# Optimization experiments

Measured on AMD Instinct MI355X. Metric: run time of the kernel, lower is better.

## Reference

```python
import jax, jax.numpy as jnp
import numpy as np

COMMITMENT = 1.0

def setup_inputs() -> dict:
    key = jax.random.key(0)
    k1, k2 = jax.random.split(key)
    x = jax.random.normal(k1, (32, 64, 64, 64), dtype=jnp.float32)       # [B, D, H, W]
    emb_w = jax.random.normal(k2, (512, 64), dtype=jnp.float32)          # [K, D] codebook
    return {"x": x, "emb_w": emb_w}

def reference(x, emb_w):
    B, D, H, W = x.shape
    K = emb_w.shape[0]
    # permute channels last and flatten: [B*H*W, D]
    xp = jnp.transpose(x, (0, 2, 3, 1))
    flat = xp.reshape(-1, D)
    # squared-distance matrix [N, K] via ||a||^2 + ||b||^2 - 2 a.b
    distances = (jnp.sum(flat * flat, axis=1, keepdims=True)
                 + jnp.sum(emb_w * emb_w, axis=1)
                 - 2.0 * jnp.matmul(flat, emb_w.T))
    encoding_flat = jnp.argmin(distances, axis=1)                        # [N]
    quantized = emb_w[encoding_flat].reshape(B, H, W, D)                 # gather
    quantized = jnp.transpose(quantized, (0, 3, 1, 2))                   # back to [B, D, H, W]
    # commitment loss: mse(stop_grad(quantized), x)
    e_latent_loss = jnp.mean((jax.lax.stop_gradient(quantized) - x) ** 2)
    loss = COMMITMENT * e_latent_loss
    # straight-through estimator
    quantized_st = x + jax.lax.stop_gradient(quantized - x)
    encoding = encoding_flat.reshape(B, H, W)
    return quantized_st, encoding, distances, loss
```

## Files before the change

### kernel.cpp

```cpp
#include <hip/hip_runtime.h>

typedef short short8 __attribute__((ext_vector_type(8)));
typedef float f32x4 __attribute__((ext_vector_type(4)));

#define EPS 0.012f

__device__ __forceinline__ unsigned short rne_bf16(float v) {
    unsigned u = __float_as_uint(v);
    unsigned r = u + 0x7FFFu + ((u >> 16) & 1u);
    return (unsigned short)(r >> 16);
}
__device__ __forceinline__ float bf16_to_f(unsigned short h) {
    return __uint_as_float(((unsigned)h) << 16);
}

#define MFMA(a,b,c) __builtin_amdgcn_mfma_f32_16x16x32_bf16((a),(b),(c),0,0,0)

__global__ __launch_bounds__(64) void prep_kernel(
    const float* __restrict__ emb, unsigned short* __restrict__ whi,
    unsigned short* __restrict__ wlo, float* __restrict__ wee)
{
    const int k = blockIdx.x * 64 + threadIdx.x;
    const float* src = emb + k * 64;
    float nrm = 0.f;
    #pragma unroll
    for (int g = 0; g < 8; ++g) {
        float4 v0 = *(const float4*)(src + g * 8);
        float4 v1 = *(const float4*)(src + g * 8 + 4);
        float vv[8] = {v0.x, v0.y, v0.z, v0.w, v1.x, v1.y, v1.z, v1.w};
        short8 h8, l8;
        #pragma unroll
        for (int i = 0; i < 8; ++i) {
            nrm = fmaf(vv[i], vv[i], nrm);
            unsigned short hb = rne_bf16(vv[i]);
            h8[i] = (short)hb;
            l8[i] = (short)rne_bf16(vv[i] - bf16_to_f(hb));
        }
        *(short8*)(whi + k * 64 + g * 8) = h8;
        *(short8*)(wlo + k * 64 + g * 8) = l8;
    }
    wee[k] = nrm;
}

#define DT 36

__global__ __launch_bounds__(256, 4) void vq_kernel(
    const float* __restrict__ x, const float* __restrict__ emb,
    const unsigned short* __restrict__ whi, const unsigned short* __restrict__ wlo,
    const float* __restrict__ wee,
    float* __restrict__ out_q, float* __restrict__ out_enc,
    float* __restrict__ out_dist, float* __restrict__ out_loss)
{
    __shared__ __align__(16) unsigned short ehi[2][32 * 64];
    __shared__ __align__(16) unsigned short elo[2][32 * 64];
    __shared__ __align__(16) float dtile[4][16 * DT];
    __shared__ float ee_s[512];
    __shared__ int   enc_s[64];
    __shared__ float red_s[4];

    const int t   = threadIdx.x;
    const int bid = blockIdx.x;
    const int n_base = bid * 64;
    const size_t xbase = (size_t)(bid >> 6) * 262144 + (size_t)(bid & 63) * 64;
    const int l  = t & 63;
    const int wv = t >> 6;

    ee_s[t]       = wee[t];
    ee_s[t + 256] = wee[t + 256];

    const int myw = wv * 16 + (l & 15);
    const int g8  = (l >> 4) * 8;
    float va[16];
    {
        const float* xp = x + xbase + myw;
        #pragma unroll
        for (int i = 0; i < 8; ++i) {
            va[i]     = xp[(size_t)(g8 + i) * 4096];
            va[8 + i] = xp[(size_t)(g8 + 32 + i) * 4096];
        }
    }
    short8 xhi0, xhi1, xlo0, xlo1;
    float xx = 0.f;
    #pragma unroll
    for (int i = 0; i < 8; ++i) {
        xx = fmaf(va[i], va[i], xx);
        xx = fmaf(va[8 + i], va[8 + i], xx);
        unsigned short hb = rne_bf16(va[i]);
        xhi0[i] = (short)hb; xlo0[i] = (short)rne_bf16(va[i] - bf16_to_f(hb));
        unsigned short hb2 = rne_bf16(va[8 + i]);
        xhi1[i] = (short)hb2; xlo1[i] = (short)rne_bf16(va[8 + i] - bf16_to_f(hb2));
    }
    xx += __shfl_xor(xx, 16, 64);
    xx += __shfl_xor(xx, 32, 64);

    short8 sh, sl;
    const int skr = t >> 3;
    const int sd0 = (t & 7) * 8;
    const int sidx = skr * 64 + (sd0 ^ ((skr & 7) << 3));
    #define STAGE_LOAD(c) {                                                    \
        sh = *(const short8*)(whi + (size_t)(((c) * 32 + skr) * 64 + sd0));    \
        sl = *(const short8*)(wlo + (size_t)(((c) * 32 + skr) * 64 + sd0));    \
    }
    #define STAGE_WRITE(bufi) {                                                \
        *(short8*)&ehi[bufi][sidx] = sh;                                       \
        *(short8*)&elo[bufi][sidx] = sl;                                       \
    }

    STAGE_LOAD(0); STAGE_WRITE(0);
    float m1 = 3.4e38f, m2 = 3.4e38f; int k1 = 0;
    const int colb = (l >> 4) * 4;
    float* dwv = dtile[wv];
    __syncthreads();

    #pragma unroll 1
    for (int c = 0; c < 16; ++c) {
        if (c < 15) STAGE_LOAD(c + 1);
        const int bufi = c & 1;
        #pragma unroll
        for (int kti = 0; kti < 2; ++kti) {
            const int krl = kti * 16 + (l & 15);
            const int sw  = (krl & 7) << 3;
            const int bix = krl * 64;
            short8 ch0 = *(short8*)&ehi[bufi][bix + (g8 ^ sw)];
            short8 ch1 = *(short8*)&ehi[bufi][bix + ((g8 + 32) ^ sw)];
            short8 cl0 = *(short8*)&elo[bufi][bix + (g8 ^ sw)];
            short8 cl1 = *(short8*)&elo[bufi][bix + ((g8 + 32) ^ sw)];
            f32x4 accA = {0.f, 0.f, 0.f, 0.f};
            f32x4 accB = {0.f, 0.f, 0.f, 0.f};
            accA = MFMA(ch0, xhi0, accA);
            accB = MFMA(ch1, xhi1, accB);
            accA = MFMA(cl0, xhi0, accA);
            accB = MFMA(cl1, xhi1, accB);
            accA = MFMA(ch0, xlo0, accA);
            accB = MFMA(ch1, xlo1, accB);
            const int kb = c * 32 + kti * 16 + colb;
            float4 ee4 = *(const float4*)&ee_s[kb];
            float eev[4] = {ee4.x, ee4.y, ee4.z, ee4.w};
            f32x4 dist4;
            #pragma unroll
            for (int r = 0; r < 4; ++r) {
                float dv = fmaf(accA[r] + accB[r], -2.f, xx + eev[r]);
                dist4[r] = dv;
                if (dv < m1) { m2 = m1; m1 = dv; k1 = kb + r; }
                else if (dv < m2) m2 = dv;
            }
            *(f32x4*)&dwv[(l & 15) * DT + (kti * 4 + (l >> 4)) * 4] = dist4;
        }
        #pragma unroll
        for (int p = 0; p < 2; ++p) {
            const int row = p * 8 + (l >> 3);
            const int k4  = (l & 7) * 4;
            f32x4 v = *(f32x4*)&dwv[row * DT + k4];
            *(f32x4*)(out_dist + (size_t)(n_base + wv * 16 + row) * 512 + c * 32 + k4) = v;
        }
        if (c < 15) STAGE_WRITE((c + 1) & 1);
        __syncthreads();
    }

    __syncthreads();

    float* drow = out_dist + (size_t)(n_base + myw) * 512;
    float bv = m1; int bk = k1;
    {
        float ov = __shfl_xor(bv, 16, 64); int ok = __shfl_xor(bk, 16, 64);
        if (ov < bv || (ov == bv && ok < bk)) { bv = ov; bk = ok; }
        ov = __shfl_xor(bv, 32, 64); ok = __shfl_xor(bk, 32, 64);
        if (ov < bv || (ov == bv && ok < bk)) { bv = ov; bk = ok; }
    }
    const float thr = bv + EPS;
    const unsigned long long gmask = 0x0001000100010001ULL << (l & 15);
    unsigned long long b1 = __ballot(m1 <= thr);
    unsigned long long b2 = __ballot(m2 <= thr);
    int enc = bk; float lossv = bv;
    if (__popcll(b1 & gmask) > 1 || (b2 & gmask) != 0ULL) {
        const float* dr   = drow + (l >> 4) * 128;
        const float* xcol = x + xbase + myw;
        double bestv = 1e300; int bestk = 0x7fffffff;
        #pragma unroll 1
        for (int c4 = 0; c4 < 32; ++c4) {
            float4 dv4 = *(const float4*)(dr + c4 * 4);
            float dvv[4] = {dv4.x, dv4.y, dv4.z, dv4.w};
            #pragma unroll 1
            for (int j = 0; j < 4; ++j) {
                if (dvv[j] <= thr) {
                    int k = (l >> 4) * 128 + c4 * 4 + j;
                    const float* er = emb + k * 64;
                    double s = 0.0;
                    #pragma unroll 4
                    for (int d = 0; d < 64; ++d) {
                        double df = (double)xcol[(size_t)d * 4096] - (double)er[d];
                        s += df * df;
                    }
                    if (s < bestv) { bestv = s; bestk = k; }
                }
            }
        }
        double ov = __shfl_xor(bestv, 16, 64); int ok = __shfl_xor(bestk, 16, 64);
        if (ov < bestv || (ov == bestv && ok < bestk)) { bestv = ov; bestk = ok; }
        ov = __shfl_xor(bestv, 32, 64); ok = __shfl_xor(bestk, 32, 64);
        if (ov < bestv || (ov == bestv && ok < bestk)) { bestv = ov; bestk = ok; }
        enc = bestk;
        if (l < 16 && enc != bk) lossv = drow[enc];
    }
    if (l < 16) {
        enc_s[myw] = enc;
        out_enc[n_base + myw] = (float)enc;
    }
    float lc = (l < 16) ? lossv : 0.f;
    #pragma unroll
    for (int m = 32; m >= 1; m >>= 1) lc += __shfl_down(lc, m, 64);
    if (l == 0) red_s[wv] = lc;
    __syncthreads();
    if (t == 0)
        atomicAdd(out_loss, (red_s[0] + red_s[1] + red_s[2] + red_s[3]) * (1.0f / 8388608.0f));

    {
        const int w  = t & 63;
        const int dg = t >> 6;
        const int e  = enc_s[w];
        const float* er = emb + e * 64 + dg * 16;
        float* qp = out_q + xbase + (size_t)(dg * 16) * 4096 + w;
        #pragma unroll
        for (int qi = 0; qi < 4; ++qi) {
            float4 q4 = *(const float4*)(er + qi * 4);
            qp[(size_t)(qi * 4 + 0) * 4096] = q4.x;
            qp[(size_t)(qi * 4 + 1) * 4096] = q4.y;
            qp[(size_t)(qi * 4 + 2) * 4096] = q4.z;
            qp[(size_t)(qi * 4 + 3) * 4096] = q4.w;
        }
    }
}

extern "C" void kernel_launch(void* const* d_in, const int* in_sizes, int n_in,
                              void* d_out, int out_size, void* d_ws, size_t ws_size,
                              hipStream_t stream) {
    const float* x   = (const float*)d_in[0];
    const float* emb = (const float*)d_in[1];

    float* out_q    = (float*)d_out;
    float* out_enc  = out_q + 8388608;
    float* out_dist = out_enc + 131072;
    float* out_loss = out_dist + 67108864;

    unsigned short* whi = (unsigned short*)d_ws;
    unsigned short* wlo = whi + 32768;
    float*          wee = (float*)(whi + 65536);

    hipMemsetAsync(out_loss, 0, sizeof(float), stream);
    prep_kernel<<<8, 64, 0, stream>>>(emb, whi, wlo, wee);
    vq_kernel<<<2048, 256, 0, stream>>>(x, emb, whi, wlo, wee,
                                        out_q, out_enc, out_dist, out_loss);
}
```

Baseline: 105.1 us.

## Fold distance epilogue into MFMA accumulators and lighten the per-chunk barrier

```diff
diff --git a/kernel.cpp b/kernel.cpp
--- a/kernel.cpp
+++ b/kernel.cpp
@@ -15,6 +15,12 @@
 }
 
 #define MFMA(a,b,c) __builtin_amdgcn_mfma_f32_16x16x32_bf16((a),(b),(c),0,0,0)
+
+#define LIGHT_BARRIER() do {                                   \
+    asm volatile("s_waitcnt lgkmcnt(0)" ::: "memory");         \
+    __builtin_amdgcn_s_barrier();                              \
+    __builtin_amdgcn_sched_barrier(0);                         \
+} while (0)
 
 __global__ __launch_bounds__(64) void prep_kernel(
     const float* __restrict__ emb, unsigned short* __restrict__ whi,
@@ -32,9 +38,10 @@
         #pragma unroll
         for (int i = 0; i < 8; ++i) {
             nrm = fmaf(vv[i], vv[i], nrm);
-            unsigned short hb = rne_bf16(vv[i]);
+            float v2 = -2.0f * vv[i];
+            unsigned short hb = rne_bf16(v2);
             h8[i] = (short)hb;
-            l8[i] = (short)rne_bf16(vv[i] - bf16_to_f(hb));
+            l8[i] = (short)rne_bf16(v2 - bf16_to_f(hb));
         }
         *(short8*)(whi + k * 64 + g * 8) = h8;
         *(short8*)(wlo + k * 64 + g * 8) = l8;
@@ -54,7 +61,7 @@
     __shared__ __align__(16) unsigned short ehi[2][32 * 64];
     __shared__ __align__(16) unsigned short elo[2][32 * 64];
     __shared__ __align__(16) float dtile[4][16 * DT];
-    __shared__ float ee_s[512];
+    __shared__ __align__(16) float ee_s[512];
     __shared__ int   enc_s[64];
     __shared__ float red_s[4];
 
@@ -92,6 +99,7 @@
     }
     xx += __shfl_xor(xx, 16, 64);
     xx += __shfl_xor(xx, 32, 64);
+    const f32x4 xx4 = {xx, xx, xx, xx};
 
     short8 sh, sl;
     const int skr = t >> 3;
@@ -112,7 +120,7 @@
     float* dwv = dtile[wv];
     __syncthreads();
 
-    #pragma unroll 1
+    #pragma unroll 2
     for (int c = 0; c < 16; ++c) {
         if (c < 15) STAGE_LOAD(c + 1);
         const int bufi = c & 1;
@@ -125,24 +133,25 @@
             short8 ch1 = *(short8*)&ehi[bufi][bix + ((g8 + 32) ^ sw)];
             short8 cl0 = *(short8*)&elo[bufi][bix + (g8 ^ sw)];
             short8 cl1 = *(short8*)&elo[bufi][bix + ((g8 + 32) ^ sw)];
-            f32x4 accA = {0.f, 0.f, 0.f, 0.f};
-            f32x4 accB = {0.f, 0.f, 0.f, 0.f};
+            const int kb = c * 32 + kti * 16 + colb;
+            f32x4 accA = *(const f32x4*)&ee_s[kb];
+            f32x4 accB = xx4;
             accA = MFMA(ch0, xhi0, accA);
             accB = MFMA(ch1, xhi1, accB);
             accA = MFMA(cl0, xhi0, accA);
             accB = MFMA(cl1, xhi1, accB);
             accA = MFMA(ch0, xlo0, accA);
             accB = MFMA(ch1, xlo1, accB);
-            const int kb = c * 32 + kti * 16 + colb;
-            float4 ee4 = *(const float4*)&ee_s[kb];
-            float eev[4] = {ee4.x, ee4.y, ee4.z, ee4.w};
             f32x4 dist4;
             #pragma unroll
             for (int r = 0; r < 4; ++r) {
-                float dv = fmaf(accA[r] + accB[r], -2.f, xx + eev[r]);
+                float dv = accA[r] + accB[r];
                 dist4[r] = dv;
-                if (dv < m1) { m2 = m1; m1 = dv; k1 = kb + r; }
-                else if (dv < m2) m2 = dv;
+                float nm2 = fmaxf(fminf(dv, m2), m1);
+                int  kidx = kb | r;
+                k1 = (dv < m1) ? kidx : k1;
+                m1 = fminf(dv, m1);
+                m2 = nm2;
             }
             *(f32x4*)&dwv[(l & 15) * DT + (kti * 4 + (l >> 4)) * 4] = dist4;
         }
@@ -154,7 +163,7 @@
             *(f32x4*)(out_dist + (size_t)(n_base + wv * 16 + row) * 512 + c * 32 + k4) = v;
         }
         if (c < 15) STAGE_WRITE((c + 1) & 1);
-        __syncthreads();
+        LIGHT_BARRIER();
     }
 
     __syncthreads();
```

New measurement: 103.3 us. No clear change (-1.6%).
